# Performance work log

Measured on AMD Instinct MI355X. Metric: run time of the kernel, lower is better.

Reference implementation:

```python
import jax, jax.numpy as jnp
import numpy as np

D_MODEL = 1024
NUM_TILES = 64
TPC = 8                      # tiles_per_cluster
NUM_CLUSTERS = NUM_TILES // TPC
GRID = 16
COMP_H = 256                 # compress hidden = d_model // 4
NUM_KNOTS = 8
EPS_LN = 1e-5


def setup_inputs() -> dict:
    key = jax.random.key(0)
    ks = jax.random.split(key, 12)
    B, T = 4, 4096
    x = jax.random.normal(ks[0], (B, T, D_MODEL), dtype=jnp.float32)
    signatures_raw = jax.random.normal(ks[1], (NUM_TILES, D_MODEL), dtype=jnp.float32) * 0.5
    knot_values = jax.nn.sigmoid(jnp.linspace(-3.0, 3.0, NUM_KNOTS).astype(jnp.float32))
    temperature = jnp.ones((1,), dtype=jnp.float32)
    # compress: Linear(d,comp_h) -> GELU -> Linear(comp_h,2) -> Tanh
    compress_w1 = jax.random.normal(ks[2], (D_MODEL, COMP_H), dtype=jnp.float32) * (1.0 / np.sqrt(D_MODEL))
    compress_b1 = jnp.zeros((COMP_H,), dtype=jnp.float32)
    compress_w2 = jax.random.normal(ks[3], (COMP_H, 2), dtype=jnp.float32) * (1.0 / np.sqrt(COMP_H))
    compress_b2 = jnp.zeros((2,), dtype=jnp.float32)
    # per-tile magnitude splines: Linear(2,grid) -> ReLU -> Linear(grid,1)
    spline_w1 = jax.random.normal(ks[4], (NUM_TILES, 2, GRID), dtype=jnp.float32) * (1.0 / np.sqrt(2.0))
    spline_b1 = jnp.zeros((NUM_TILES, GRID), dtype=jnp.float32)
    spline_w2 = jax.random.normal(ks[5], (NUM_TILES, GRID, 1), dtype=jnp.float32) * (1.0 / np.sqrt(GRID))
    spline_b2 = jnp.zeros((NUM_TILES, 1), dtype=jnp.float32)
    directions = jax.random.normal(ks[6], (NUM_TILES, D_MODEL), dtype=jnp.float32) * 0.02
    norm_gamma = jnp.ones((D_MODEL,), dtype=jnp.float32)
    norm_beta = jnp.zeros((D_MODEL,), dtype=jnp.float32)
    output_scale = jnp.ones((1,), dtype=jnp.float32) * 0.1
    return dict(x=x, signatures_raw=signatures_raw, knot_values=knot_values,
                temperature=temperature, compress_w1=compress_w1, compress_b1=compress_b1,
                compress_w2=compress_w2, compress_b2=compress_b2, spline_w1=spline_w1,
                spline_b1=spline_b1, spline_w2=spline_w2, spline_b2=spline_b2,
                directions=directions, norm_gamma=norm_gamma, norm_beta=norm_beta,
                output_scale=output_scale)


def _calibrate(scores, knots, temperature):
    # ScoreCalibrationSpline: sigmoid -> linear interpolation over knots
    K = knots.shape[0]
    normalized = jax.nn.sigmoid(scores / (temperature[0] + 1e-6))
    idx_float = normalized * (K - 1)
    idx_low = jnp.clip(idx_float.astype(jnp.int32), 0, K - 2)
    idx_high = idx_low + 1
    t = idx_float - idx_low.astype(scores.dtype)
    val_low = knots[idx_low]
    val_high = knots[idx_high]
    return val_low + t * (val_high - val_low)


def _forward(x, signatures_raw, knot_values, temperature, compress_w1, compress_b1,
             compress_w2, compress_b2, spline_w1, spline_b1, spline_w2, spline_b2,
             directions, norm_gamma, norm_beta, output_scale):
    B, T, D = x.shape
    xf = x.reshape(-1, D)  # [N, D]

    # ternary quantized signatures with straight-through estimator
    q = jnp.where(signatures_raw > 0.3, 1.0,
                  jnp.where(signatures_raw < -0.3, -1.0, 0.0)).astype(signatures_raw.dtype)
    sigs = signatures_raw + jax.lax.stop_gradient(q - signatures_raw)  # [NT, D]

    # hierarchical routing: cluster signatures = sign(mean of member sigs)
    cluster_sigs = jnp.sign(sigs.reshape(NUM_CLUSTERS, TPC, D).mean(axis=1))  # [NC, D]
    cluster_scores = xf @ cluster_sigs.T                                       # [N, NC]
    cluster_gates = _calibrate(cluster_scores, knot_values, temperature)
    cluster_idx = jnp.argmax(cluster_gates, axis=-1)                           # [N]

    # within-cluster tile selection (clusters are contiguous blocks of tiles)
    tile_scores = xf @ sigs.T                                                  # [N, NT]
    tile_gates = _calibrate(tile_scores, knot_values, temperature)
    gates_by_cluster = tile_gates.reshape(-1, NUM_CLUSTERS, TPC)
    sel_gates = jnp.take_along_axis(gates_by_cluster, cluster_idx[:, None, None],
                                    axis=1)[:, 0, :]                            # [N, TPC]
    local_idx = jnp.argmax(sel_gates, axis=-1)
    tile_idx = cluster_idx * TPC + local_idx                                    # [N]

    # compress to 2D spline coordinates
    h = jax.nn.gelu(xf @ compress_w1 + compress_b1, approximate=False)
    comp = jnp.tanh(h @ compress_w2 + compress_b2)                              # [N, 2]

    # batched per-token tiny spline MLP (gather selected tile's weights)
    w1 = spline_w1[tile_idx]                                                    # [N, 2, G]
    b1 = spline_b1[tile_idx]                                                    # [N, G]
    hh = jax.nn.relu(jnp.einsum('ni,nig->ng', comp, w1) + b1)                   # [N, G]
    w2 = spline_w2[tile_idx]                                                    # [N, G, 1]
    b2 = spline_b2[tile_idx]                                                    # [N, 1]
    mag = jnp.einsum('ng,ngo->no', hh, w2) + b2                                 # [N, 1]

    ffn_out = mag * directions[tile_idx] * output_scale[0]                      # [N, D]

    # residual + LayerNorm (dropout in eval mode = identity)
    y = xf + ffn_out
    mu = y.mean(axis=-1, keepdims=True)
    var = ((y - mu) ** 2).mean(axis=-1, keepdims=True)
    y = (y - mu) / jnp.sqrt(var + EPS_LN) * norm_gamma + norm_beta
    return y.reshape(B, T, D)


def reference(x, signatures_raw, knot_values, temperature, compress_w1, compress_b1,
              compress_w2, compress_b2, spline_w1, spline_b1, spline_w2, spline_b2,
              directions, norm_gamma, norm_beta, output_scale):
    return _forward(x, signatures_raw, knot_values, temperature, compress_w1, compress_b1,
                    compress_w2, compress_b2, spline_w1, spline_b1, spline_w2, spline_b2,
                    directions, norm_gamma, norm_beta, output_scale)
```

## Files before the change

### kernel.cpp

```cpp
#include <hip/hip_runtime.h>
#include <hip/hip_bf16.h>
#include <cmath>

#define N_TOK 16384
#define DM    1024
#define CH    256
#define SGRID 16
#define NTP   24

typedef __attribute__((ext_vector_type(8))) short short8;
typedef __attribute__((ext_vector_type(4))) float floatx4;

__device__ __forceinline__ unsigned short f2bf(float f) {
  union { float f; unsigned int u; } v; v.f = f;
  unsigned int r = v.u + 0x7FFFu + ((v.u >> 16) & 1u);
  return (unsigned short)(r >> 16);
}

__device__ __forceinline__ short8 cvt8(float4 u, float4 v) {
  union { short8 s; __hip_bfloat162 h[4]; } r;
  r.h[0] = __float22bfloat162_rn(make_float2(u.x, u.y));
  r.h[1] = __float22bfloat162_rn(make_float2(u.z, u.w));
  r.h[2] = __float22bfloat162_rn(make_float2(v.x, v.y));
  r.h[3] = __float22bfloat162_rn(make_float2(v.z, v.w));
  return r.s;
}

__device__ __forceinline__ float bf2f(unsigned short b) {
  union { unsigned int u; float f; } v; v.u = ((unsigned int)b) << 16; return v.f;
}

__device__ __forceinline__ float calibrate(float s, const float* __restrict__ kn, float temp_eff) {
  float nrm = 1.0f / (1.0f + expf(-s / temp_eff));
  float idxf = nrm * 7.0f;
  int il = (int)idxf; if (il > 6) il = 6;
  float tt = idxf - (float)il;
  float lo = kn[il], hi = kn[il + 1];
  return lo + tt * (hi - lo);
}

__global__ __launch_bounds__(256) void prep_kernel(
    const float* __restrict__ sig_raw, const float* __restrict__ w1,
    unsigned short* __restrict__ wsB) {
  __shared__ float Wt[32][260];
  __shared__ float St[64][33];
  int kk = blockIdx.x, tid = threadIdx.x;
  {
    int r = tid >> 3, c0 = (tid & 7) * 32;
    const float* src = w1 + (size_t)(kk * 32 + r) * CH + c0;
#pragma unroll
    for (int i = 0; i < 8; ++i)
      *(float4*)(&Wt[r][c0 + 4 * i]) = *(const float4*)(src + 4 * i);
  }
  {
    int t = tid >> 2, c0 = (tid & 3) * 8;
    const float* src = sig_raw + (size_t)t * DM + kk * 32 + c0;
#pragma unroll
    for (int i = 0; i < 8; ++i) {
      float rr = src[i];
      St[t][c0 + i] = (rr > 0.3f) ? 1.f : ((rr < -0.3f) ? -1.f : 0.f);
    }
  }
  __syncthreads();
#pragma unroll
  for (int i = 0; i < 4; ++i) {
    int idx = i * 256 + tid;
    int nt = idx >> 6, lane = idx & 63;
    int q = lane >> 4, l = lane & 15;
    short8 v;
#pragma unroll
    for (int j = 0; j < 8; ++j) v[j] = (short)f2bf(Wt[q * 8 + j][nt * 16 + l]);
    *(short8*)(wsB + ((size_t)(kk * NTP + nt) * 64 + lane) * 8) = v;
  }
#pragma unroll
  for (int i = 0; i < 2; ++i) {
    int idx = i * 256 + tid;
    if (idx < 320) {
      int nt = 16 + (idx >> 6), lane = idx & 63;
      int q = lane >> 4, l = lane & 15;
      int n = nt * 16 + l;
      short8 v;
#pragma unroll
      for (int j = 0; j < 8; ++j) {
        int kl = q * 8 + j;
        float val = 0.f;
        if (n < 264) {
          float s = 0.f;
#pragma unroll
          for (int m = 0; m < 8; ++m) s += St[(n - 256) * 8 + m][kl];
          val = (s > 0.f) ? 1.f : ((s < 0.f) ? -1.f : 0.f);
        } else if (n < 328) {
          val = St[n - 264][kl];
        }
        v[j] = (short)f2bf(val);
      }
      *(short8*)(wsB + ((size_t)(kk * NTP + nt) * 64 + lane) * 8) = v;
    }
  }
}


#define LOADK(kk, bv, aav)                                                  \
  {                                                                         \
    const char* bp = bBase + (size_t)(kk) * (NTP * 1024);                   \
    _Pragma("unroll") for (int s = 0; s < 5; ++s)                           \
        bv[s] = *(const short8*)(bp + s * 4096);                            \
    if (w3 == 0) bv[5] = *(const short8*)(bp + 20 * 1024);                  \
    aav = *(const short8*)(Xsh + arow + (((unsigned)((kk) * 4 + quad) ^ sw) << 3)); \
  }

#define COMPUTE(bv, aav)                                                    \
  {                                                                         \
    _Pragma("unroll") for (int s = 0; s < 5; ++s)                           \
      acc[s] = __builtin_amdgcn_mfma_f32_16x16x32_bf16(aav, bv[s], acc[s], 0, 0, 0); \
    if (w3 == 0)                                                            \
      acc[5] = __builtin_amdgcn_mfma_f32_16x16x32_bf16(aav, bv[5], acc[5], 0, 0, 0); \
  }

__global__ __launch_bounds__(512, 4) void fused_kernel(
    const float* __restrict__ x, const unsigned short* __restrict__ wsB,
    const float* __restrict__ b1, const float* __restrict__ w2,
    const float* __restrict__ b2, const float* __restrict__ knots,
    const float* __restrict__ temperature, const float* __restrict__ sw1,
    const float* __restrict__ sb1, const float* __restrict__ sw2,
    const float* __restrict__ sb2, const float* __restrict__ dirs,
    const float* __restrict__ gma, const float* __restrict__ bta,
    const float* __restrict__ oscale, float* __restrict__ out) {
  __shared__ unsigned short Xsh[32 * 1024];
  __shared__ float Ssc[32][73];
  __shared__ float Psh[2][4][16][2];
  __shared__ float ScaleS[32];
  __shared__ int   TidxS[32];

  int tid = threadIdx.x;
  int wave = tid >> 6, lane = tid & 63, quad = lane >> 4, l15 = lane & 15;
  int w3 = wave & 3, h = wave >> 2;
  int m0 = blockIdx.x * 32;

  {
    const float* base = x + (size_t)m0 * DM;
#pragma unroll
    for (int i2 = 0; i2 < 8; ++i2) {
      int cg = tid + 512 * i2;
      float4 p = *(const float4*)(base + cg * 8);
      float4 q = *(const float4*)(base + cg * 8 + 4);
      int row = cg >> 7, cir = cg & 127;
      int pos = cir ^ (row & 7);
      *(short8*)(Xsh + row * 1024 + pos * 8) = cvt8(p, q);
    }
  }
  __syncthreads();

  floatx4 acc[6];
#pragma unroll
  for (int s = 0; s < 6; ++s) acc[s] = (floatx4){0.f, 0.f, 0.f, 0.f};

  const char* bBase = (const char*)wsB + w3 * 1024 + lane * 16;
  int arow = (h * 16 + l15) * 1024;
  unsigned sw = (unsigned)(l15 & 7);

  short8 bA[6], bB_[6], aA, aB_;
  LOADK(0, bA, aA);
#pragma unroll 1
  for (int kk = 0; kk < 30; kk += 2) {
    LOADK(kk + 1, bB_, aB_);
    COMPUTE(bA, aA);
    LOADK(kk + 2, bA, aA);
    COMPUTE(bB_, aB_);
  }
  LOADK(31, bB_, aB_);
  COMPUTE(bA, aA);
  COMPUTE(bB_, aB_);

#pragma unroll
  for (int r = 0; r < 4; ++r) {
    int row = h * 16 + quad * 4 + r;
    Ssc[row][w3 * 16 + l15] = acc[4][r];
    if (w3 == 0 && l15 < 8) Ssc[row][64 + l15] = acc[5][r];
  }

  float p0[4] = {0.f, 0.f, 0.f, 0.f}, p1[4] = {0.f, 0.f, 0.f, 0.f};
#pragma unroll
  for (int s = 0; s < 4; ++s) {
    int col = (w3 + 4 * s) * 16 + l15;
    float b1c = b1[col], w20 = w2[2 * col], w21 = w2[2 * col + 1];
#pragma unroll
    for (int r = 0; r < 4; ++r) {
      float hh = acc[s][r] + b1c;
      hh = 0.5f * hh * (1.0f + erff(hh * 0.7071067811865475f));
      p0[r] += hh * w20;
      p1[r] += hh * w21;
    }
  }
#pragma unroll
  for (int m = 1; m < 16; m <<= 1)
#pragma unroll
    for (int r = 0; r < 4; ++r) {
      p0[r] += __shfl_xor(p0[r], m);
      p1[r] += __shfl_xor(p1[r], m);
    }
  if (l15 == 0) {
#pragma unroll
    for (int r = 0; r < 4; ++r) {
      Psh[h][w3][quad * 4 + r][0] = p0[r];
      Psh[h][w3][quad * 4 + r][1] = p1[r];
    }
  }
  __syncthreads();

  if (tid < 32) {
    int row = tid, h2 = row >> 4, r16 = row & 15;
    float s0 = b2[0], s1 = b2[1];
#pragma unroll
    for (int j = 0; j < 4; ++j) {
      s0 += Psh[h2][j][r16][0];
      s1 += Psh[h2][j][r16][1];
    }
    float c0 = tanhf(s0), c1 = tanhf(s1);

    float temp_eff = temperature[0] + 1e-6f;
    int cid = 0; float best = -1e30f;
#pragma unroll
    for (int c = 0; c < 8; ++c) {
      float g = calibrate(Ssc[row][c], knots, temp_eff);
      if (g > best) { best = g; cid = c; }
    }
    int lidx = 0; best = -1e30f;
#pragma unroll
    for (int j = 0; j < 8; ++j) {
      float g = calibrate(Ssc[row][8 + cid * 8 + j], knots, temp_eff);
      if (g > best) { best = g; lidx = j; }
    }
    int t = cid * 8 + lidx;

    float mag = sb2[t];
#pragma unroll
    for (int g2 = 0; g2 < SGRID; ++g2) {
      float hv = c0 * sw1[t * 32 + g2] + c1 * sw1[t * 32 + 16 + g2] + sb1[t * 16 + g2];
      hv = fmaxf(hv, 0.f);
      mag += hv * sw2[t * 16 + g2];
    }
    ScaleS[row] = mag * oscale[0];
    TidxS[row] = t;
  }
  __syncthreads();

#pragma unroll 1
  for (int rr = 0; rr < 4; ++rr) {
    int row = wave * 4 + rr;
    int r7 = row & 7;
    float scale = ScaleS[row];
    const float* dr = dirs + (size_t)TidxS[row] * DM + lane * 16;
    const unsigned short* xrow = Xsh + row * 1024;
    short8 h0 = *(const short8*)(xrow + (unsigned)((2 * lane) ^ r7) * 8);
    short8 h1 = *(const short8*)(xrow + (unsigned)((2 * lane + 1) ^ r7) * 8);
    float fv[16];
    float ssum = 0.f, ssq = 0.f;
#pragma unroll
    for (int i = 0; i < 4; ++i) {
      float4 d4 = *(const float4*)(dr + 4 * i);
      float xa = bf2f((unsigned short)((i < 2 ? h0[i * 4 + 0] : h1[(i - 2) * 4 + 0])));
      float xb = bf2f((unsigned short)((i < 2 ? h0[i * 4 + 1] : h1[(i - 2) * 4 + 1])));
      float xc = bf2f((unsigned short)((i < 2 ? h0[i * 4 + 2] : h1[(i - 2) * 4 + 2])));
      float xd = bf2f((unsigned short)((i < 2 ? h0[i * 4 + 3] : h1[(i - 2) * 4 + 3])));
      fv[4 * i + 0] = xa + scale * d4.x;
      fv[4 * i + 1] = xb + scale * d4.y;
      fv[4 * i + 2] = xc + scale * d4.z;
      fv[4 * i + 3] = xd + scale * d4.w;
      ssum += fv[4 * i + 0] + fv[4 * i + 1] + fv[4 * i + 2] + fv[4 * i + 3];
      ssq += fv[4 * i + 0] * fv[4 * i + 0] + fv[4 * i + 1] * fv[4 * i + 1]
           + fv[4 * i + 2] * fv[4 * i + 2] + fv[4 * i + 3] * fv[4 * i + 3];
    }
#pragma unroll
    for (int m = 1; m < 64; m <<= 1) {
      ssum += __shfl_xor(ssum, m);
      ssq += __shfl_xor(ssq, m);
    }
    float mu = ssum * (1.0f / 1024.0f);
    float var = ssq * (1.0f / 1024.0f) - mu * mu;
    float inv = rsqrtf(var + 1e-5f);
    float* orow = out + (size_t)(m0 + row) * DM + lane * 16;
    const float* gp = gma + lane * 16;
    const float* bp2 = bta + lane * 16;
#pragma unroll
    for (int i = 0; i < 4; ++i) {
      float4 g4 = *(const float4*)(gp + 4 * i);
      float4 b4 = *(const float4*)(bp2 + 4 * i);
      float4 o;
      o.x = (fv[4 * i + 0] - mu) * inv * g4.x + b4.x;
      o.y = (fv[4 * i + 1] - mu) * inv * g4.y + b4.y;
      o.z = (fv[4 * i + 2] - mu) * inv * g4.z + b4.z;
      o.w = (fv[4 * i + 3] - mu) * inv * g4.w + b4.w;
      *(float4*)(orow + 4 * i) = o;
    }
  }
}

extern "C" void kernel_launch(void* const* d_in, const int* in_sizes, int n_in,
                              void* d_out, int out_size, void* d_ws, size_t ws_size,
                              hipStream_t stream) {
  const float* x      = (const float*)d_in[0];
  const float* sigraw = (const float*)d_in[1];
  const float* knots  = (const float*)d_in[2];
  const float* temp   = (const float*)d_in[3];
  const float* cw1    = (const float*)d_in[4];
  const float* cb1    = (const float*)d_in[5];
  const float* cw2    = (const float*)d_in[6];
  const float* cb2    = (const float*)d_in[7];
  const float* sw1    = (const float*)d_in[8];
  const float* sb1    = (const float*)d_in[9];
  const float* sw2    = (const float*)d_in[10];
  const float* sb2    = (const float*)d_in[11];
  const float* dirs   = (const float*)d_in[12];
  const float* gma    = (const float*)d_in[13];
  const float* bta    = (const float*)d_in[14];
  const float* oscale = (const float*)d_in[15];
  float* out = (float*)d_out;

  unsigned short* wsB = (unsigned short*)d_ws;

  hipLaunchKernelGGL(prep_kernel, dim3(32), dim3(256), 0, stream,
                     sigraw, cw1, wsB);
  hipLaunchKernelGGL(fused_kernel, dim3(N_TOK / 32), dim3(512), 0, stream,
                     x, wsB, cb1, cw2, cb2, knots, temp,
                     sw1, sb1, sw2, sb2, dirs, gma, bta, oscale, out);
}
```

Baseline: 184.2 us.

## Retile fused kernel to 64-token blocks with per-wave column tiles

Each block now handles 64 tokens with 1024 threads. Each of the 16 waves owns one 16-column slice of the compress hidden layer across four 16-row M tiles, and waves 0-4 also compute the signature-score columns. Weight fragments are reused across four A tiles, which cuts global B-load traffic per token. The cost is doubled LDS use (128KB for X), which limits occupancy to one block per CU. The change also leaves a dead duplicate GELU loop and a larger shuffle reduction.

```diff
diff --git a/kernel.cpp b/kernel.cpp
--- a/kernel.cpp
+++ b/kernel.cpp
@@ -100,48 +100,50 @@
 }
 
 
-#define LOADK(kk, bv, aav)                                                  \
+#define LOADK(kk, b0, b1, av)                                               \
   {                                                                         \
     const char* bp = bBase + (size_t)(kk) * (NTP * 1024);                   \
-    _Pragma("unroll") for (int s = 0; s < 5; ++s)                           \
-        bv[s] = *(const short8*)(bp + s * 4096);                            \
-    if (w3 == 0) bv[5] = *(const short8*)(bp + 20 * 1024);                  \
-    aav = *(const short8*)(Xsh + arow + (((unsigned)((kk) * 4 + quad) ^ sw) << 3)); \
-  }
-
-#define COMPUTE(bv, aav)                                                    \
+    b0 = *(const short8*)(bp);                                              \
+    if (wave < 5) b1 = *(const short8*)(bp + 16384);                        \
+    unsigned cpos = ((unsigned)((kk) * 4 + quad) ^ sw) << 3;                \
+    _Pragma("unroll") for (int mt = 0; mt < 4; ++mt)                        \
+        av[mt] = *(const short8*)(Xsh + mt * 16384 + arow + cpos);          \
+  }
+
+#define COMPUTE(b0, b1, av)                                                 \
   {                                                                         \
-    _Pragma("unroll") for (int s = 0; s < 5; ++s)                           \
-      acc[s] = __builtin_amdgcn_mfma_f32_16x16x32_bf16(aav, bv[s], acc[s], 0, 0, 0); \
-    if (w3 == 0)                                                            \
-      acc[5] = __builtin_amdgcn_mfma_f32_16x16x32_bf16(aav, bv[5], acc[5], 0, 0, 0); \
-  }
-
-__global__ __launch_bounds__(512, 4) void fused_kernel(
+    _Pragma("unroll") for (int mt = 0; mt < 4; ++mt)                        \
+      acc0[mt] = __builtin_amdgcn_mfma_f32_16x16x32_bf16(av[mt], b0, acc0[mt], 0, 0, 0); \
+    if (wave < 5) {                                                         \
+      _Pragma("unroll") for (int mt = 0; mt < 4; ++mt)                      \
+        acc1[mt] = __builtin_amdgcn_mfma_f32_16x16x32_bf16(av[mt], b1, acc1[mt], 0, 0, 0); \
+    }                                                                       \
+  }
+
+__global__ __launch_bounds__(1024, 4) void fused_kernel(
     const float* __restrict__ x, const unsigned short* __restrict__ wsB,
-    const float* __restrict__ b1, const float* __restrict__ w2,
+    const float* __restrict__ b1v, const float* __restrict__ w2,
     const float* __restrict__ b2, const float* __restrict__ knots,
     const float* __restrict__ temperature, const float* __restrict__ sw1,
     const float* __restrict__ sb1, const float* __restrict__ sw2,
     const float* __restrict__ sb2, const float* __restrict__ dirs,
     const float* __restrict__ gma, const float* __restrict__ bta,
     const float* __restrict__ oscale, float* __restrict__ out) {
-  __shared__ unsigned short Xsh[32 * 1024];
-  __shared__ float Ssc[32][73];
-  __shared__ float Psh[2][4][16][2];
-  __shared__ float ScaleS[32];
-  __shared__ int   TidxS[32];
+  __shared__ unsigned short Xsh[64 * 1024];
+  __shared__ float Ssc[64][73];
+  __shared__ float Psh[16][64][2];
+  __shared__ float ScaleS[64];
+  __shared__ int   TidxS[64];
 
   int tid = threadIdx.x;
   int wave = tid >> 6, lane = tid & 63, quad = lane >> 4, l15 = lane & 15;
-  int w3 = wave & 3, h = wave >> 2;
-  int m0 = blockIdx.x * 32;
+  int m0 = blockIdx.x * 64;
 
   {
     const float* base = x + (size_t)m0 * DM;
 #pragma unroll
     for (int i2 = 0; i2 < 8; ++i2) {
-      int cg = tid + 512 * i2;
+      int cg = tid + 1024 * i2;
       float4 p = *(const float4*)(base + cg * 8);
       float4 q = *(const float4*)(base + cg * 8 + 4);
       int row = cg >> 7, cir = cg & 127;
@@ -151,70 +153,99 @@
   }
   __syncthreads();
 
-  floatx4 acc[6];
-#pragma unroll
-  for (int s = 0; s < 6; ++s) acc[s] = (floatx4){0.f, 0.f, 0.f, 0.f};
-
-  const char* bBase = (const char*)wsB + w3 * 1024 + lane * 16;
-  int arow = (h * 16 + l15) * 1024;
+  floatx4 acc0[4], acc1[4];
+#pragma unroll
+  for (int mt = 0; mt < 4; ++mt) {
+    acc0[mt] = (floatx4){0.f, 0.f, 0.f, 0.f};
+    acc1[mt] = (floatx4){0.f, 0.f, 0.f, 0.f};
+  }
+
+  const char* bBase = (const char*)wsB + wave * 1024 + lane * 16;
+  int arow = l15 * 1024;
   unsigned sw = (unsigned)(l15 & 7);
 
-  short8 bA[6], bB_[6], aA, aB_;
-  LOADK(0, bA, aA);
+  short8 bA0, bA1, bB0, bB1, aA[4], aB_[4];
+  LOADK(0, bA0, bA1, aA);
 #pragma unroll 1
   for (int kk = 0; kk < 30; kk += 2) {
-    LOADK(kk + 1, bB_, aB_);
-    COMPUTE(bA, aA);
-    LOADK(kk + 2, bA, aA);
-    COMPUTE(bB_, aB_);
-  }
-  LOADK(31, bB_, aB_);
-  COMPUTE(bA, aA);
-  COMPUTE(bB_, aB_);
-
-#pragma unroll
-  for (int r = 0; r < 4; ++r) {
-    int row = h * 16 + quad * 4 + r;
-    Ssc[row][w3 * 16 + l15] = acc[4][r];
-    if (w3 == 0 && l15 < 8) Ssc[row][64 + l15] = acc[5][r];
-  }
-
-  float p0[4] = {0.f, 0.f, 0.f, 0.f}, p1[4] = {0.f, 0.f, 0.f, 0.f};
-#pragma unroll
-  for (int s = 0; s < 4; ++s) {
-    int col = (w3 + 4 * s) * 16 + l15;
-    float b1c = b1[col], w20 = w2[2 * col], w21 = w2[2 * col + 1];
-#pragma unroll
-    for (int r = 0; r < 4; ++r) {
-      float hh = acc[s][r] + b1c;
-      hh = 0.5f * hh * (1.0f + erff(hh * 0.7071067811865475f));
-      p0[r] += hh * w20;
-      p1[r] += hh * w21;
-    }
-  }
-#pragma unroll
-  for (int m = 1; m < 16; m <<= 1)
-#pragma unroll
-    for (int r = 0; r < 4; ++r) {
-      p0[r] += __shfl_xor(p0[r], m);
-      p1[r] += __shfl_xor(p1[r], m);
-    }
-  if (l15 == 0) {
-#pragma unroll
-    for (int r = 0; r < 4; ++r) {
-      Psh[h][w3][quad * 4 + r][0] = p0[r];
-      Psh[h][w3][quad * 4 + r][1] = p1[r];
+    LOADK(kk + 1, bB0, bB1, aB_);
+    COMPUTE(bA0, bA1, aA);
+    LOADK(kk + 2, bA0, bA1, aA);
+    COMPUTE(bB0, bB1, aB_);
+  }
+  LOADK(31, bB0, bB1, aB_);
+  COMPUTE(bA0, bA1, aA);
+  COMPUTE(bB0, bB1, aB_);
+
+  if (wave < 5) {
+    int sc = wave * 16 + l15;
+    if (sc < 72) {
+#pragma unroll
+      for (int mt = 0; mt < 4; ++mt)
+#pragma unroll
+        for (int r = 0; r < 4; ++r)
+          Ssc[mt * 16 + quad * 4 + r][sc] = acc1[mt][r];
+    }
+  }
+
+  {
+    int col = wave * 16 + l15;
+    float b1c = b1v[col], w20 = w2[2 * col], w21 = w2[2 * col + 1];
+    float p0[4], p1[4];
+#pragma unroll
+    for (int mt = 0; mt < 4; ++mt) { p0[mt] = 0.f; p1[mt] = 0.f; }
+#pragma unroll
+    for (int mt = 0; mt < 4; ++mt)
+#pragma unroll
+      for (int r = 0; r < 4; ++r) {
+        float hh = acc0[mt][r] + b1c;
+        hh = 0.5f * hh * (1.0f + erff(hh * 0.7071067811865475f));
+        if (r == 0) { p0[mt] += hh * w20; p1[mt] += hh * w21; }
+        else if (r == 1) { p0[mt] = p0[mt]; p1[mt] = p1[mt]; p0[mt] += 0.f; p1[mt] += 0.f;
+        }
+      }
+  }
+  {
+    int col = wave * 16 + l15;
+    float b1c = b1v[col], w20 = w2[2 * col], w21 = w2[2 * col + 1];
+    float q0[4][4], q1[4][4];
+#pragma unroll
+    for (int mt = 0; mt < 4; ++mt)
+#pragma unroll
+      for (int r = 0; r < 4; ++r) {
+        float hh = acc0[mt][r] + b1c;
+        hh = 0.5f * hh * (1.0f + erff(hh * 0.7071067811865475f));
+        q0[mt][r] = hh * w20;
+        q1[mt][r] = hh * w21;
+      }
+#pragma unroll
+    for (int m = 1; m < 16; m <<= 1)
+#pragma unroll
+      for (int mt = 0; mt < 4; ++mt)
+#pragma unroll
+        for (int r = 0; r < 4; ++r) {
+          q0[mt][r] += __shfl_xor(q0[mt][r], m);
+          q1[mt][r] += __shfl_xor(q1[mt][r], m);
+        }
+    if (l15 == 0) {
+#pragma unroll
+      for (int mt = 0; mt < 4; ++mt)
+#pragma unroll
+        for (int r = 0; r < 4; ++r) {
+          Psh[wave][mt * 16 + quad * 4 + r][0] = q0[mt][r];
+          Psh[wave][mt * 16 + quad * 4 + r][1] = q1[mt][r];
+        }
     }
   }
   __syncthreads();
 
-  if (tid < 32) {
-    int row = tid, h2 = row >> 4, r16 = row & 15;
+  if (tid < 64) {
+    int row = tid;
     float s0 = b2[0], s1 = b2[1];
 #pragma unroll
-    for (int j = 0; j < 4; ++j) {
-      s0 += Psh[h2][j][r16][0];
-      s1 += Psh[h2][j][r16][1];
+    for (int j = 0; j < 16; ++j) {
+      s0 += Psh[j][row][0];
+      s1 += Psh[j][row][1];
     }
     float c0 = tanhf(s0), c1 = tanhf(s1);
 
@@ -321,7 +352,7 @@
 
   hipLaunchKernelGGL(prep_kernel, dim3(32), dim3(256), 0, stream,
                      sigraw, cw1, wsB);
-  hipLaunchKernelGGL(fused_kernel, dim3(N_TOK / 32), dim3(512), 0, stream,
+  hipLaunchKernelGGL(fused_kernel, dim3(N_TOK / 64), dim3(1024), 0, stream,
                      x, wsB, cb1, cw2, cb2, knots, temp,
                      sw1, sb1, sw2, sb2, dirs, gma, bta, oscale, out);
 }
```

Result: faster. 176.1 us (-4.4%).
